# Performance work log

Measured on AMD Instinct MI355X. Metric: run time of the kernel, lower is better.

Reference implementation:

```python
import jax, jax.numpy as jnp
import numpy as np

SEQ_LEN, BZ, D_IN = 512, 64, 1024
HIDDEN, D_OUT, NUM_LANG = 256, 1024, 16


def setup_inputs() -> dict:
    key = jax.random.key(0)
    ks = jax.random.split(key, 6)
    x = jax.random.normal(ks[0], (SEQ_LEN, BZ, D_IN), dtype=jnp.float32)
    lang_ids = jax.random.randint(ks[1], (BZ,), 0, NUM_LANG, dtype=jnp.int64)
    # Per-language 2-layer MLP params, stacked over the language axis.
    # Stored as [in, out] so y = x @ W + b (same math as torch Linear's x @ W.T + b).
    s1 = 1.0 / np.sqrt(D_IN)
    s2 = 1.0 / np.sqrt(HIDDEN)
    W1 = jax.random.uniform(ks[2], (NUM_LANG, D_IN, HIDDEN), jnp.float32, -s1, s1)
    b1 = jax.random.uniform(ks[3], (NUM_LANG, HIDDEN), jnp.float32, -s1, s1)
    W2 = jax.random.uniform(ks[4], (NUM_LANG, HIDDEN, D_OUT), jnp.float32, -s2, s2)
    b2 = jax.random.uniform(ks[5], (NUM_LANG, D_OUT), jnp.float32, -s2, s2)
    return {"x": x, "lang_ids": lang_ids, "W1": W1, "b1": b1, "W2": W2, "b2": b2}


def reference(x, lang_ids, W1, b1, W2, b2):
    # Gather each batch element's expert weights, then do batched GEMMs.
    # Equivalent to the torch loop (dispatch -> per-expert MLP -> combine),
    # without redundant gather/scatter passes.
    W1g = W1[lang_ids]            # [bz, d_in, hidden]
    b1g = b1[lang_ids]            # [bz, hidden]
    W2g = W2[lang_ids]            # [bz, hidden, d_out]
    b2g = b2[lang_ids]            # [bz, d_out]
    h = jnp.einsum('sbd,bdh->sbh', x, W1g) + b1g[None, :, :]
    h = jax.nn.relu(h)
    y = jnp.einsum('sbh,bho->sbo', h, W2g) + b2g[None, :, :]
    return y
```

## Files before the change

### kernel.cpp

```cpp
#include <hip/hip_runtime.h>

#define SEQ 512
#define BZ  64
#define DIN 1024
#define HID 256
#define DOUT 1024
#define NLANG 16

typedef __attribute__((ext_vector_type(8))) __bf16 bf16x8;
typedef __attribute__((ext_vector_type(4))) float f32x4;

__device__ __forceinline__ unsigned short f2bf(float f) {
    return __builtin_bit_cast(unsigned short, (__bf16)f);
}
__device__ __forceinline__ unsigned int f2bf_pack(float lo, float hi) {
    return (unsigned int)f2bf(lo) | ((unsigned int)f2bf(hi) << 16);
}

template<int K, int N>
__global__ __launch_bounds__(256)
void prep_frags(const float* __restrict__ src, unsigned short* __restrict__ dst) {
    constexpr int K32 = K / 32, N16 = N / 16;
    const int gid = blockIdx.x * 256 + threadIdx.x;
    const int l   = gid & 63;
    const int f   = gid >> 6;
    const int k32 = f & (K32 - 1);
    const int n16 = (f / K32) & (N16 - 1);
    const int lid = f / (K32 * N16);
    const float* s = src + ((long)lid * K + k32 * 32 + (l >> 4) * 8) * N + n16 * 16 + (l & 15);
    unsigned short o[8];
#pragma unroll
    for (int j = 0; j < 8; ++j) o[j] = f2bf(s[(long)j * N]);
    uint4 v;
    v.x = (unsigned int)o[0] | ((unsigned int)o[1] << 16);
    v.y = (unsigned int)o[2] | ((unsigned int)o[3] << 16);
    v.z = (unsigned int)o[4] | ((unsigned int)o[5] << 16);
    v.w = (unsigned int)o[6] | ((unsigned int)o[7] << 16);
    *(uint4*)(dst + (long)gid * 8) = v;
}

__global__ __launch_bounds__(512, 2)
void fused_mlp(const float* __restrict__ x,
               const unsigned short* __restrict__ W1f,
               const float* __restrict__ b1,
               const unsigned short* __restrict__ W2f,
               const float* __restrict__ b2,
               const int* __restrict__ lang,
               float* __restrict__ y) {
    __shared__ unsigned short sA[2][64 * 64];
    __shared__ unsigned short sH[64 * 256];
    char* cH = (char*)sH;

    const int b  = blockIdx.x;
    const int st = blockIdx.y;
    const int t  = threadIdx.x;
    const int l  = t & 63;
    const int w  = t >> 6;
    const int lid = lang[b];
    const int s0  = st * 64;
    const long xstride = (long)BZ * DIN;
    const float* xb = x + (long)s0 * xstride + (long)b * DIN;

    const f32x4 z4 = {0.f, 0.f, 0.f, 0.f};

    f32x4 acc1[4][2];
#pragma unroll
    for (int mi = 0; mi < 4; ++mi)
#pragma unroll
        for (int ni = 0; ni < 2; ++ni) acc1[mi][ni] = z4;

    float4 xr[2];
#define LOADX(KT)                                                                  \
    {                                                                              \
        _Pragma("unroll")                                                          \
        for (int j = 0; j < 2; ++j) {                                              \
            int u = t + 512 * j, m = u >> 4, c4 = u & 15;                          \
            xr[j] = *(const float4*)(xb + (long)m * xstride + (KT) * 64 + c4 * 4); \
        }                                                                          \
    }
#define WRITEX(BUF)                                                               \
    {                                                                             \
        char* cA = (char*)sA[BUF];                                                \
        _Pragma("unroll")                                                         \
        for (int j = 0; j < 2; ++j) {                                             \
            int u = t + 512 * j, m = u >> 4, c4 = u & 15;                         \
            uint2 p;                                                              \
            p.x = f2bf_pack(xr[j].x, xr[j].y);                                    \
            p.y = f2bf_pack(xr[j].z, xr[j].w);                                    \
            *(uint2*)(cA + (((m * 128) + c4 * 8) ^ ((m & 7) << 4))) = p;          \
        }                                                                         \
    }

    const unsigned short* w1p = W1f + (((long)lid * 16 + w * 2) * 32) * 512 + (long)l * 8;

    float bvv[2];
#pragma unroll
    for (int ni = 0; ni < 2; ++ni)
        bvv[ni] = b1[lid * HID + w * 32 + ni * 16 + (l & 15)];

    LOADX(0);
    WRITEX(0);
    bf16x8 bvp[2][2];
#pragma unroll
    for (int ni = 0; ni < 2; ++ni)
        bvp[0][ni] = __builtin_bit_cast(bf16x8, *(const uint4*)(w1p + (long)ni * 16384));
    __syncthreads();

    for (int kt = 0; kt < 16; ++kt) {
        if (kt < 15) LOADX(kt + 1);
        char* cA = (char*)sA[kt & 1];
#pragma unroll
        for (int ks = 0; ks < 2; ++ks) {
            const int k32 = kt * 2 + ks;
            if (k32 < 31) {
#pragma unroll
                for (int ni = 0; ni < 2; ++ni)
                    bvp[(k32 + 1) & 1][ni] = __builtin_bit_cast(bf16x8,
                        *(const uint4*)(w1p + (long)ni * 16384 + (k32 + 1) * 512));
            }
            bf16x8 av[4];
#pragma unroll
            for (int mi = 0; mi < 4; ++mi) {
                int row = mi * 16 + (l & 15);
                int ch  = ks * 4 + (l >> 4);
                av[mi] = __builtin_bit_cast(bf16x8,
                    *(const uint4*)(cA + row * 128 + ((ch ^ (row & 7)) << 4)));
            }
#pragma unroll
            for (int mi = 0; mi < 4; ++mi)
#pragma unroll
                for (int ni = 0; ni < 2; ++ni)
                    acc1[mi][ni] = __builtin_amdgcn_mfma_f32_16x16x32_bf16(
                        av[mi], bvp[k32 & 1][ni], acc1[mi][ni], 0, 0, 0);
        }
        if (kt < 15) WRITEX((kt & 1) ^ 1);
        __syncthreads();
    }

#pragma unroll
    for (int mi = 0; mi < 4; ++mi)
#pragma unroll
        for (int r = 0; r < 4; ++r) {
            int row = mi * 16 + (l >> 4) * 4 + r;
#pragma unroll
            for (int ni = 0; ni < 2; ++ni) {
                int col = w * 32 + ni * 16 + (l & 15);
                float v = acc1[mi][ni][r] + bvv[ni];
                v = v > 0.f ? v : 0.f;
                *(unsigned short*)(cH + row * 512 + (((col >> 3) ^ (row & 7)) << 4)
                                   + (col & 7) * 2) = f2bf(v);
            }
        }
    __syncthreads();

    const unsigned short* w2p = W2f + (((long)lid * 64 + w * 8) * 8) * 512 + (long)l * 8;

    bf16x8 pv[2][4];
#pragma unroll
    for (int ni = 0; ni < 4; ++ni)
        pv[0][ni] = __builtin_bit_cast(bf16x8, *(const uint4*)(w2p + (long)ni * 4096));

    f32x4 acc[4][4];
    float b2v[4];
#pragma unroll
    for (int s = 0; s < 16; ++s) {
        const int nc = s >> 3, ks = s & 7, cur = s & 1;
        if (ks == 0) {
#pragma unroll
            for (int mi = 0; mi < 4; ++mi)
#pragma unroll
                for (int ni = 0; ni < 4; ++ni) acc[mi][ni] = z4;
#pragma unroll
            for (int ni = 0; ni < 4; ++ni)
                b2v[ni] = b2[lid * DOUT + w * 128 + nc * 64 + ni * 16 + (l & 15)];
        }
        if (s < 15) {
            const int ns = s + 1, nq = (ns >> 3) * 4, ks1 = ns & 7;
#pragma unroll
            for (int ni = 0; ni < 4; ++ni)
                pv[cur ^ 1][ni] = __builtin_bit_cast(bf16x8,
                    *(const uint4*)(w2p + (long)(nq + ni) * 4096 + ks1 * 512));
        }
        bf16x8 av2[4];
#pragma unroll
        for (int mi = 0; mi < 4; ++mi) {
            int row = mi * 16 + (l & 15);
            int ch  = ks * 4 + (l >> 4);
            av2[mi] = __builtin_bit_cast(bf16x8,
                *(const uint4*)(cH + row * 512 + ((ch ^ (row & 7)) << 4)));
        }
#pragma unroll
        for (int mi = 0; mi < 4; ++mi)
#pragma unroll
            for (int ni = 0; ni < 4; ++ni)
                acc[mi][ni] = __builtin_amdgcn_mfma_f32_16x16x32_bf16(
                    av2[mi], pv[cur][ni], acc[mi][ni], 0, 0, 0);
        if (ks == 7) {
#pragma unroll
            for (int mi = 0; mi < 4; ++mi)
#pragma unroll
                for (int r = 0; r < 4; ++r) {
                    int row = mi * 16 + (l >> 4) * 4 + r;
#pragma unroll
                    for (int ni = 0; ni < 4; ++ni) {
                        int col = w * 128 + nc * 64 + ni * 16 + (l & 15);
                        y[((long)(s0 + row) * BZ + b) * DOUT + col] =
                            acc[mi][ni][r] + b2v[ni];
                    }
                }
        }
    }
#undef LOADX
#undef WRITEX
}

extern "C" void kernel_launch(void* const* d_in, const int* in_sizes, int n_in,
                              void* d_out, int out_size, void* d_ws, size_t ws_size,
                              hipStream_t stream) {
    const float* x    = (const float*)d_in[0];
    const int*   lang = (const int*)d_in[1];
    const float* W1   = (const float*)d_in[2];
    const float* b1   = (const float*)d_in[3];
    const float* W2   = (const float*)d_in[4];
    const float* b2   = (const float*)d_in[5];
    float* y = (float*)d_out;

    unsigned short* W1f = (unsigned short*)d_ws;
    unsigned short* W2f = (unsigned short*)((char*)d_ws + (size_t)NLANG * HID * DIN * 2);

    prep_frags<DIN, HID><<<2048, 256, 0, stream>>>(W1, W1f);
    prep_frags<HID, DOUT><<<2048, 256, 0, stream>>>(W2, W2f);

    fused_mlp<<<dim3(BZ, SEQ / 64), 512, 0, stream>>>(x, W1f, b1, W2f, b2, lang, y);
}
```

Baseline: 95.98 us.

## Split fused MLP into two kernels with hidden activations staged in workspace

Splits the fused two-layer kernel into a layer-1 kernel that writes the swizzled bf16 hidden tile to global workspace and a layer-2 kernel that loads it into LDS with global_load_lds. Each kernel has a smaller register and LDS footprint, so the launch bounds are raised to allow more blocks per CU. The cost is an extra launch plus a global round trip for the hidden activations, about 16 MB written and then read back.

```diff
diff --git a/kernel.cpp b/kernel.cpp
--- a/kernel.cpp
+++ b/kernel.cpp
@@ -15,6 +15,11 @@
 }
 __device__ __forceinline__ unsigned int f2bf_pack(float lo, float hi) {
     return (unsigned int)f2bf(lo) | ((unsigned int)f2bf(hi) << 16);
+}
+__device__ __forceinline__ void gload_lds16(const unsigned short* g, unsigned short* l) {
+    __builtin_amdgcn_global_load_lds(
+        (const __attribute__((address_space(1))) unsigned int*)g,
+        (__attribute__((address_space(3))) unsigned int*)l, 16, 0, 0);
 }
 
 template<int K, int N>
@@ -39,14 +44,12 @@
     *(uint4*)(dst + (long)gid * 8) = v;
 }
 
-__global__ __launch_bounds__(512, 2)
-void fused_mlp(const float* __restrict__ x,
-               const unsigned short* __restrict__ W1f,
-               const float* __restrict__ b1,
-               const unsigned short* __restrict__ W2f,
-               const float* __restrict__ b2,
-               const int* __restrict__ lang,
-               float* __restrict__ y) {
+__global__ __launch_bounds__(512, 6)
+void mlp_l1(const float* __restrict__ x,
+            const unsigned short* __restrict__ W1f,
+            const float* __restrict__ b1,
+            const int* __restrict__ lang,
+            unsigned short* __restrict__ h_ws) {
     __shared__ unsigned short sA[2][64 * 64];
     __shared__ unsigned short sH[64 * 256];
     char* cH = (char*)sH;
@@ -153,12 +156,48 @@
         }
     __syncthreads();
 
+    uint4* hw = (uint4*)(h_ws + ((long)(b * 8 + st)) * 16384);
+    const uint4* sq = (const uint4*)sH;
+#pragma unroll
+    for (int j = 0; j < 4; ++j)
+        hw[t + 512 * j] = sq[t + 512 * j];
+#undef LOADX
+#undef WRITEX
+}
+
+__global__ __launch_bounds__(512, 4)
+void mlp_l2(const unsigned short* __restrict__ h_ws,
+            const unsigned short* __restrict__ W2f,
+            const float* __restrict__ b2,
+            const int* __restrict__ lang,
+            float* __restrict__ y) {
+    __shared__ unsigned short sH[64 * 256];
+    char* cH = (char*)sH;
+
+    const int b  = blockIdx.x;
+    const int st = blockIdx.y;
+    const int t  = threadIdx.x;
+    const int l  = t & 63;
+    const int w  = t >> 6;
+    const int lid = lang[b];
+    const int s0  = st * 64;
+
+    const unsigned short* hw = h_ws + ((long)(b * 8 + st)) * 16384;
+#pragma unroll
+    for (int j = 0; j < 4; ++j) {
+        int seg = w * 4 + j;
+        gload_lds16(hw + seg * 512 + l * 8, sH + seg * 512);
+    }
+
     const unsigned short* w2p = W2f + (((long)lid * 64 + w * 8) * 8) * 512 + (long)l * 8;
 
+    const f32x4 z4 = {0.f, 0.f, 0.f, 0.f};
     bf16x8 pv[2][4];
 #pragma unroll
     for (int ni = 0; ni < 4; ++ni)
         pv[0][ni] = __builtin_bit_cast(bf16x8, *(const uint4*)(w2p + (long)ni * 4096));
+
+    __syncthreads();
 
     f32x4 acc[4][4];
     float b2v[4];
@@ -210,8 +249,6 @@
                 }
         }
     }
-#undef LOADX
-#undef WRITEX
 }
 
 extern "C" void kernel_launch(void* const* d_in, const int* in_sizes, int n_in,
@@ -227,9 +264,12 @@
 
     unsigned short* W1f = (unsigned short*)d_ws;
     unsigned short* W2f = (unsigned short*)((char*)d_ws + (size_t)NLANG * HID * DIN * 2);
+    unsigned short* hws = (unsigned short*)((char*)d_ws + (size_t)NLANG * HID * DIN * 2
+                                                       + (size_t)NLANG * DOUT * HID * 2);
 
     prep_frags<DIN, HID><<<2048, 256, 0, stream>>>(W1, W1f);
     prep_frags<HID, DOUT><<<2048, 256, 0, stream>>>(W2, W2f);
 
-    fused_mlp<<<dim3(BZ, SEQ / 64), 512, 0, stream>>>(x, W1f, b1, W2f, b2, lang, y);
-}
+    mlp_l1<<<dim3(BZ, SEQ / 64), 512, 0, stream>>>(x, W1f, b1, lang, hws);
+    mlp_l2<<<dim3(BZ, SEQ / 64), 512, 0, stream>>>(hws, W2f, b2, lang, y);
+}
```

New measurement: 165.7 us. +72.7%, slower.
